# Kernel tuning notes

Hardware: AMD Instinct MI355X
Metric: run time of the kernel (lower is better)

The kernel has to match this reference:

```python
import jax, jax.numpy as jnp
import numpy as np

K = 3
KK = K * K
EPS = 1e-5


def conv2d(x, w, b, pad):
    y = jax.lax.conv_general_dilated(x, w, (1, 1), [(pad, pad), (pad, pad)],
                                     dimension_numbers=("NCHW", "OIHW", "NCHW"))
    return y + b[None, :, None, None]


def bn(x, g, b, m, v):
    inv = g / jnp.sqrt(v + EPS)
    return x * inv[None, :, None, None] + (b - m * inv)[None, :, None, None]


def deform_sample(x, dy, dx):
    # x: [B,C,H,W]; dy,dx: [B,KK,H,W] -> sampled [B,C,KK,H,W] (bilinear, zeros outside)
    B, C, H, W = x.shape
    k = jnp.arange(K, dtype=x.dtype) - 1.0  # pad=1, dilation=1, stride=1
    ky = jnp.repeat(k, K)  # [KK] row offsets
    kx = jnp.tile(k, K)    # [KK] col offsets
    hh = jnp.arange(H, dtype=x.dtype)
    ww = jnp.arange(W, dtype=x.dtype)
    py = hh[None, :, None] + ky[:, None, None] + dy  # [B,KK,H,W]
    px = ww[None, None, :] + kx[:, None, None] + dx

    def sample_one(img, py, px):
        y0f = jnp.floor(py); x0f = jnp.floor(px)
        wy = py - y0f; wx = px - x0f
        y0 = y0f.astype(jnp.int32); x0 = x0f.astype(jnp.int32)

        def gather(yi, xi, w):
            valid = (yi >= 0) & (yi < H) & (xi >= 0) & (xi < W)
            yc = jnp.clip(yi, 0, H - 1); xc = jnp.clip(xi, 0, W - 1)
            v = img[:, yc, xc]  # [C,KK,H,W]
            return v * (w * valid)[None]

        return (gather(y0, x0, (1 - wy) * (1 - wx)) +
                gather(y0, x0 + 1, (1 - wy) * wx) +
                gather(y0 + 1, x0, wy * (1 - wx)) +
                gather(y0 + 1, x0 + 1, wy * wx))

    return jax.vmap(sample_one)(x, py, px)


def setup_inputs() -> dict:
    key = jax.random.key(0)
    ks = jax.random.split(key, 16)
    B, C, H, W = 8, 256, 64, 64
    d = {
        "feature": jax.random.normal(ks[0], (B, C, H, W), jnp.float32),
        "p1_w": jax.random.normal(ks[1], (C, C, 1, 1), jnp.float32) * 0.05,
        "p1_b": jax.random.normal(ks[2], (C,), jnp.float32) * 0.05,
        "bn1_g": jax.random.normal(ks[3], (C,), jnp.float32) * 0.1 + 1.0,
        "bn1_b": jax.random.normal(ks[4], (C,), jnp.float32) * 0.05,
        "bn1_m": jax.random.normal(ks[5], (C,), jnp.float32) * 0.05,
        "bn1_v": jax.random.uniform(ks[6], (C,), jnp.float32) + 0.5,
        "off_w": jax.random.normal(ks[7], (3 * KK, 2 * C, K, K), jnp.float32) * 0.01,
        "off_b": jax.random.normal(ks[8], (3 * KK,), jnp.float32) * 0.01,
        "dcn_w": jax.random.normal(ks[9], (C, C, K, K), jnp.float32) * 0.05,
        "dcn_b": jax.random.normal(ks[10], (C,), jnp.float32) * 0.05,
        "bn2_g": jax.random.normal(ks[11], (C,), jnp.float32) * 0.1 + 1.0,
        "bn2_b": jax.random.normal(ks[12], (C,), jnp.float32) * 0.05,
        "bn2_m": jax.random.normal(ks[13], (C,), jnp.float32) * 0.05,
        "bn2_v": jax.random.uniform(ks[14], (C,), jnp.float32) + 0.5,
    }
    return d


def reference(feature, p1_w, p1_b, bn1_g, bn1_b, bn1_m, bn1_v,
              off_w, off_b, dcn_w, dcn_b, bn2_g, bn2_b, bn2_m, bn2_v):
    flipped = feature[..., ::-1]                      # flip last (W) axis
    proj = bn(conv2d(feature, p1_w, p1_b, 0), bn1_g, bn1_b, bn1_m, bn1_v)
    # DCNv2: offsets/mask from concat(flipped, proj)
    concat = jnp.concatenate([flipped, proj], axis=1)
    off = conv2d(concat, off_w, off_b, 1)             # [B,27,H,W]
    dy = off[:, :KK]
    dx = off[:, KK:2 * KK]
    mask = jax.nn.sigmoid(off[:, 2 * KK:])            # [B,KK,H,W]
    sampled = deform_sample(flipped, dy, dx)          # [B,C,KK,H,W]
    O = dcn_w.shape[0]
    y = jnp.einsum("bckhw,ock->bohw", sampled * mask[:, None], dcn_w.reshape(O, -1, KK))
    y = y + dcn_b[None, :, None, None]
    y = bn(y, bn2_g, bn2_b, bn2_m, bn2_v)
    return jax.nn.relu(proj + y)
```

## Files before the change

### kernel.cpp

```cpp
#include <hip/hip_runtime.h>
#include <hip/hip_bf16.h>
#include <math.h>

typedef __attribute__((ext_vector_type(8))) short short8;
typedef __attribute__((ext_vector_type(4))) short short4v;
typedef __attribute__((ext_vector_type(4))) float f32x4;

__device__ __forceinline__ float bs2f(short s){
    union { unsigned u; float f; } x; x.u = ((unsigned)(unsigned short)s) << 16; return x.f;
}
__device__ __forceinline__ short f2bs(float f){
    union { float f; unsigned u; } x; x.f = f;
    unsigned r = x.u + 0x7fff + ((x.u >> 16) & 1);
    return (short)(r >> 16);
}
__device__ __forceinline__ float blo(unsigned u){
    union { unsigned u; float f; } x; x.u = u << 16; return x.f;
}
__device__ __forceinline__ float bhi(unsigned u){
    union { unsigned u; float f; } x; x.u = u & 0xffff0000u; return x.f;
}
__device__ __forceinline__ unsigned pack2(float lo, float hi){
    union { float f; unsigned u; } a, b; a.f = lo; b.f = hi;
    unsigned rl = a.u + 0x7fff + ((a.u >> 16) & 1);
    unsigned rh = b.u + 0x7fff + ((b.u >> 16) & 1);
    return (rl >> 16) | (rh & 0xffff0000u);
}
__device__ __forceinline__ void gl2lds16(const void* g, void* l){
    __builtin_amdgcn_global_load_lds(
        (const __attribute__((address_space(1))) void*)g,
        (__attribute__((address_space(3))) void*)l, 16, 0, 0);
}

#define XPB ((size_t)66*66*512)


__global__ void k_prep(const float* __restrict__ p1_w, const float* __restrict__ p1_b,
                       const float* __restrict__ bn1_g, const float* __restrict__ bn1_b,
                       const float* __restrict__ bn1_m, const float* __restrict__ bn1_v,
                       const float* __restrict__ off_w,
                       const float* __restrict__ dcn_w, const float* __restrict__ dcn_b,
                       const float* __restrict__ bn2_g, const float* __restrict__ bn2_b,
                       const float* __restrict__ bn2_m, const float* __restrict__ bn2_v,
                       short* __restrict__ p1_wb, short* __restrict__ Woffb,
                       short* __restrict__ Wbf,
                       float* __restrict__ bias1f, float* __restrict__ inv2f,
                       float* __restrict__ bias2f, unsigned* __restrict__ XpadU)
{
    int blk = blockIdx.x, t = threadIdx.x;
    if (blk == 0) {
        float inv1 = bn1_g[t] / sqrtf(bn1_v[t] + 1e-5f);
        bias1f[t] = p1_b[t] * inv1 + bn1_b[t] - bn1_m[t] * inv1;
        float inv2 = bn2_g[t] / sqrtf(bn2_v[t] + 1e-5f);
        inv2f[t] = inv2;
        bias2f[t] = dcn_b[t] * inv2 + bn2_b[t] - bn2_m[t] * inv2;
    } else if (blk <= 256) {
        int ci = blk - 1;
        float inv1 = bn1_g[t] / sqrtf(bn1_v[t] + 1e-5f);
        p1_wb[t*256 + ci] = f2bs(p1_w[t*256 + ci] * inv1);
    } else if (blk <= 2560) {
        int ck = blk - 257;
        int c = ck / 9, tap = ck % 9;
        Wbf[t*2304 + tap*256 + c] = f2bs(dcn_w[t*2304 + ck]);
    } else if (blk <= 7168) {
        int e = blk - 2561;
        if (t < 32) {
            int tap = e >> 9, ci = e & 511;
            float v = off_w[((t < 27) ? t : 0)*4608 + ci*9 + tap];
            Woffb[t*4608 + e] = (t < 27) ? f2bs(v) : (short)0;
        }
    } else {
        int hb = blk - 7169;
        int b = hb / 260, i = hb % 260;
        int y, x;
        if (i < 66)       { y = 0;  x = i; }
        else if (i < 132) { y = 65; x = i - 66; }
        else { int j = i - 132; y = 1 + (j >> 1); x = (j & 1) * 65; }
        XpadU[((size_t)(b*66 + y)*66 + x)*256 + t] = 0u;
    }
}

__global__ void k_featT(const float* __restrict__ feature, short* __restrict__ Xpad)
{
    __shared__ float tile[64][65];
    int bb = blockIdx.x;
    int cg = bb & 3, h = (bb >> 2) & 63, b = bb >> 8;
    int c0 = cg * 64;
    int t = threadIdx.x;
    int lw = t & 63, li = t >> 6;
    #pragma unroll
    for (int j = 0; j < 16; ++j) {
        int cl = j*4 + li;
        tile[cl][63 - lw] = feature[((b*256 + c0 + cl)*64 + h)*64 + lw];
    }
    __syncthreads();
    #pragma unroll
    for (int j = 0; j < 16; ++j) {
        int wl = j*4 + li;
        Xpad[((size_t)(b*66 + h+1)*66 + (wl+1))*512 + c0 + lw] = f2bs(tile[lw][wl]);
    }
}

__global__ __launch_bounds__(512, 4) void k_projm(
    short* Xpad, const short* __restrict__ p1_wb, const float* __restrict__ bias1f)
{
    __shared__ short Ash[256*32];
    __shared__ short Bsh[64*32];
    int bid = blockIdx.x;
    int b = bid >> 6, h = bid & 63;
    int t = threadIdx.x;
    int lane = t & 63, w = t >> 6;
    int ln = lane & 15, q = lane >> 4;
    int r16 = lane >> 2;
    int sq  = (lane & 3) ^ ((lane >> 3) & 3);
    int rq  = (q ^ ((ln >> 1) & 3)) * 8;
    size_t rowbase = (size_t)(b*66 + h + 1)*66;

    f32x4 acc[2][4] = {};
    for (int kt = 0; kt < 8; ++kt) {
        int kcol = kt*32 + sq*8;
        #pragma unroll
        for (int i = 0; i < 2; ++i) {
            int row = w*32 + i*16 + r16;
            gl2lds16(p1_wb + (size_t)row*256 + kcol, Ash + (w*32 + i*16)*32);
        }
        if (w < 4) {
            int x = w*16 + r16;
            gl2lds16(Xpad + (rowbase + (64 - x))*512 + kcol, Bsh + (w*16)*32);
        }
        __syncthreads();
        short8 af[2], bfr[4];
        #pragma unroll
        for (int i = 0; i < 2; ++i)
            af[i] = *(const short8*)&Ash[(w*32 + i*16 + ln)*32 + rq];
        #pragma unroll
        for (int j = 0; j < 4; ++j)
            bfr[j] = *(const short8*)&Bsh[(j*16 + ln)*32 + rq];
        #pragma unroll
        for (int i = 0; i < 2; ++i)
            #pragma unroll
            for (int j = 0; j < 4; ++j)
                acc[i][j] = __builtin_amdgcn_mfma_f32_16x16x32_bf16(af[i], bfr[j], acc[i][j], 0, 0, 0);
        __syncthreads();
    }
    #pragma unroll
    for (int i = 0; i < 2; ++i) {
        int ob = w*32 + i*16 + q*4;
        #pragma unroll
        for (int j = 0; j < 4; ++j) {
            int x = j*16 + ln;
            size_t xb = (rowbase + x + 1)*512 + 256 + ob;
            short4v st;
            st.x = f2bs(acc[i][j][0] + bias1f[ob]);
            st.y = f2bs(acc[i][j][1] + bias1f[ob+1]);
            st.z = f2bs(acc[i][j][2] + bias1f[ob+2]);
            st.w = f2bs(acc[i][j][3] + bias1f[ob+3]);
            *(short4v*)&Xpad[xb] = st;
        }
    }
}

__global__ __launch_bounds__(512, 4) void k_offm(
    const short* __restrict__ Xpad, const short* __restrict__ Woffb,
    const float* __restrict__ off_b, float* __restrict__ offv)
{
    __shared__ short Ash[4][32*32];
    __shared__ short Bsh[4][64*32];
    int bid = blockIdx.x;
    int b = bid >> 6, h = bid & 63;
    int t = threadIdx.x;
    int lane = t & 63, w = t >> 6;
    int ln = lane & 15, q = lane >> 4;
    int wr = w >> 2, wc = w & 3;
    int r16 = lane >> 2;
    int sq  = (lane & 3) ^ ((lane >> 3) & 3);
    int rq  = (q ^ ((ln >> 1) & 3)) * 8;
    const short* xb = Xpad + (size_t)b*XPB;

    f32x4 acc = {};
    for (int it = 0; it < 36; ++it) {
        int tap = it >> 2, c0 = (it & 3) << 7;
        int dy = tap/3 - 1, dx = tap%3 - 1;
        #pragma unroll
        for (int s = 0; s < 4; ++s) {
            int cc = c0 + s*32 + sq*8;
            if (w < 4) {
                int row = w*16 + r16;
                const short* gB = xb + ((size_t)(h + 1 + dy)*66 + (row + dx + 1))*512 + cc;
                gl2lds16(gB, &Bsh[s][(w*16)*32]);
            } else if (w < 6) {
                int row = (w-4)*16 + r16;
                const short* gA = Woffb + (size_t)row*4608 + tap*512 + cc;
                gl2lds16(gA, &Ash[s][((w-4)*16)*32]);
            }
        }
        __syncthreads();
        #pragma unroll
        for (int s = 0; s < 4; ++s) {
            short8 af  = *(const short8*)&Ash[s][(wr*16 + ln)*32 + rq];
            short8 bfr = *(const short8*)&Bsh[s][(wc*16 + ln)*32 + rq];
            acc = __builtin_amdgcn_mfma_f32_16x16x32_bf16(af, bfr, acc, 0, 0, 0);
        }
        __syncthreads();
    }
    int x = wc*16 + ln;
    #pragma unroll
    for (int r = 0; r < 4; ++r) {
        int oc = wr*16 + q*4 + r;
        if (oc < 27)
            offv[((b*27 + oc)*64 + h)*64 + x] = acc[r] + off_b[oc];
    }
}

__global__ __launch_bounds__(512, 4) void k_gemm(
    const short* __restrict__ Xpad,
    const short* __restrict__ Wbf,
    const float* __restrict__ offv,
    const float* __restrict__ inv2f, const float* __restrict__ bias2f,
    float* __restrict__ out)
{
    __shared__ __align__(16) short Ash[2][256*32];
    __shared__ __align__(16) short Bsh[2][64*32];
    __shared__ int   c_off[576*4];
    __shared__ float c_w[576*4];
    int bid = blockIdx.x;
    int b = bid & 7, h = bid >> 3;
    int t = threadIdx.x;
    int lane = t & 63, w = t >> 6;
    int ln = lane & 15, q = lane >> 4;
    int r16 = lane >> 2;
    int sq  = (lane & 3) ^ ((lane >> 3) & 3);
    int rq  = (q ^ ((ln >> 1) & 3)) * 8;

    for (int e = t; e < 576; e += 512) {
        int p = e / 9, k = e % 9;
        int base = (b*27)*4096 + h*64 + p;
        float dy = offv[base + k*4096];
        float dx = offv[base + (9+k)*4096];
        float ms = offv[base + (18+k)*4096];
        ms = 1.f / (1.f + expf(-ms));
        float py = (float)h + (float)(k/3 - 1) + dy;
        float px = (float)p + (float)(k%3 - 1) + dx;
        float y0f = floorf(py), x0f = floorf(px);
        float wy = py - y0f, wx = px - x0f;
        int y0 = (int)y0f, x0 = (int)x0f;
        int y1 = y0 + 1, x1 = x0 + 1;
        float vy0 = (y0 >= 0 && y0 < 64) ? 1.f : 0.f;
        float vy1 = (y1 >= 0 && y1 < 64) ? 1.f : 0.f;
        float vx0 = (x0 >= 0 && x0 < 64) ? 1.f : 0.f;
        float vx1 = (x1 >= 0 && x1 < 64) ? 1.f : 0.f;
        int y0c = min(max(y0,0),63), y1c = min(max(y1,0),63);
        int x0c = min(max(x0,0),63), x1c = min(max(x1,0),63);
        c_off[e*4+0] = ((y0c+1)*66 + x0c+1)*128;
        c_off[e*4+1] = ((y0c+1)*66 + x1c+1)*128;
        c_off[e*4+2] = ((y1c+1)*66 + x0c+1)*128;
        c_off[e*4+3] = ((y1c+1)*66 + x1c+1)*128;
        c_w[e*4+0] = ms * (1.f-wy)*(1.f-wx) * vy0*vx0;
        c_w[e*4+1] = ms * (1.f-wy)*wx       * vy0*vx1;
        c_w[e*4+2] = ms * wy*(1.f-wx)       * vy1*vx0;
        c_w[e*4+3] = ms * wy*wx             * vy1*vx1;
    }
    __syncthreads();

    const uint2* fT = (const uint2*)Xpad + (size_t)b*(XPB/4);
    int pr = t >> 3;
    int jo = t & 7;
    int pe4 = pr*9*4;
    short* bdst = &Bsh[jo >> 2][pr*32 + (((jo & 3) ^ ((pr >> 1) & 3)) << 3)];

    f32x4 acc[2][4] = {};
    int4 co = *(const int4*)&c_off[pe4];
    uint4 u0 = *(const uint4*)(fT + co.x + jo*2);
    uint4 u1 = *(const uint4*)(fT + co.y + jo*2);
    uint4 u2 = *(const uint4*)(fT + co.z + jo*2);
    uint4 u3 = *(const uint4*)(fT + co.w + jo*2);

    #pragma unroll 2
    for (int kc2 = 0; kc2 < 36; ++kc2) {
        int tap = kc2 >> 2;
        int kn = kc2 < 35 ? kc2 + 1 : 35;
        int4 cn = *(const int4*)&c_off[pe4 + (kn >> 2)*4];
        int cin = ((kn & 3) << 4) + jo*2;
        uint4 v0 = *(const uint4*)(fT + cn.x + cin);
        uint4 v1 = *(const uint4*)(fT + cn.y + cin);
        uint4 v2 = *(const uint4*)(fT + cn.z + cin);
        uint4 v3 = *(const uint4*)(fT + cn.w + cin);
        #pragma unroll
        for (int s = 0; s < 2; ++s) {
            int kcol = (kc2*2 + s)*32 + sq*8;
            #pragma unroll
            for (int i = 0; i < 2; ++i) {
                int row = w*32 + i*16 + r16;
                gl2lds16(Wbf + (size_t)row*2304 + kcol, &Ash[s][(w*32 + i*16)*32]);
            }
        }
        const float4 cw = *(const float4*)&c_w[pe4 + tap*4];
        float g0 = cw.x*blo(u0.x) + cw.y*blo(u1.x) + cw.z*blo(u2.x) + cw.w*blo(u3.x);
        float g1 = cw.x*bhi(u0.x) + cw.y*bhi(u1.x) + cw.z*bhi(u2.x) + cw.w*bhi(u3.x);
        float g2 = cw.x*blo(u0.y) + cw.y*blo(u1.y) + cw.z*blo(u2.y) + cw.w*blo(u3.y);
        float g3 = cw.x*bhi(u0.y) + cw.y*bhi(u1.y) + cw.z*bhi(u2.y) + cw.w*bhi(u3.y);
        float g4 = cw.x*blo(u0.z) + cw.y*blo(u1.z) + cw.z*blo(u2.z) + cw.w*blo(u3.z);
        float g5 = cw.x*bhi(u0.z) + cw.y*bhi(u1.z) + cw.z*bhi(u2.z) + cw.w*bhi(u3.z);
        float g6 = cw.x*blo(u0.w) + cw.y*blo(u1.w) + cw.z*blo(u2.w) + cw.w*blo(u3.w);
        float g7 = cw.x*bhi(u0.w) + cw.y*bhi(u1.w) + cw.z*bhi(u2.w) + cw.w*bhi(u3.w);
        uint4 pk;
        pk.x = pack2(g0, g1); pk.y = pack2(g2, g3);
        pk.z = pack2(g4, g5); pk.w = pack2(g6, g7);
        *(uint4*)bdst = pk;
        u0 = v0; u1 = v1; u2 = v2; u3 = v3;
        __syncthreads();
        #pragma unroll
        for (int s = 0; s < 2; ++s) {
            short8 af[2], bfr[4];
            #pragma unroll
            for (int i = 0; i < 2; ++i)
                af[i] = *(const short8*)&Ash[s][(w*32 + i*16 + ln)*32 + rq];
            #pragma unroll
            for (int jj = 0; jj < 4; ++jj)
                bfr[jj] = *(const short8*)&Bsh[s][(jj*16 + ln)*32 + rq];
            #pragma unroll
            for (int i = 0; i < 2; ++i)
                #pragma unroll
                for (int jj = 0; jj < 4; ++jj)
                    acc[i][jj] = __builtin_amdgcn_mfma_f32_16x16x32_bf16(af[i], bfr[jj], acc[i][jj], 0, 0, 0);
        }
        __syncthreads();
    }

    #pragma unroll
    for (int i = 0; i < 2; ++i) {
        int ob = w*32 + i*16 + q*4;
        #pragma unroll
        for (int jj = 0; jj < 4; ++jj) {
            int p = jj*16 + ln;
            size_t xb = ((size_t)(b*66 + h + 1)*66 + p + 1)*512 + 256 + ob;
            short4v prr = *(const short4v*)&Xpad[xb];
            #pragma unroll
            for (int r = 0; r < 4; ++r) {
                int o = ob + r;
                size_t idx = ((size_t)(b*256 + o))*4096 + h*64 + p;
                float rs = bs2f(((const short*)&prr)[r]);
                float v = rs + acc[i][jj][r]*inv2f[o] + bias2f[o];
                out[idx] = v < 0.f ? 0.f : v;
            }
        }
    }
}

extern "C" void kernel_launch(void* const* d_in, const int* in_sizes, int n_in,
                              void* d_out, int out_size, void* d_ws, size_t ws_size,
                              hipStream_t stream)
{
    const float* feature = (const float*)d_in[0];
    const float* p1_w  = (const float*)d_in[1];
    const float* p1_b  = (const float*)d_in[2];
    const float* bn1_g = (const float*)d_in[3];
    const float* bn1_b = (const float*)d_in[4];
    const float* bn1_m = (const float*)d_in[5];
    const float* bn1_v = (const float*)d_in[6];
    const float* off_w = (const float*)d_in[7];
    const float* off_b = (const float*)d_in[8];
    const float* dcn_w = (const float*)d_in[9];
    const float* dcn_b = (const float*)d_in[10];
    const float* bn2_g = (const float*)d_in[11];
    const float* bn2_b = (const float*)d_in[12];
    const float* bn2_m = (const float*)d_in[13];
    const float* bn2_v = (const float*)d_in[14];

    float* ws = (float*)d_ws;
    short* Xpad   = (short*)ws;
    float* offbuf = ws + 8921088;
    short* p1_wb  = (short*)(ws + 9805824);
    short* Woffb  = (short*)(ws + 9838592);
    short* Wbf    = (short*)(ws + 9912320);
    float* bias1f = ws + 10207232;
    float* inv2f  = ws + 10207488;
    float* bias2f = ws + 10207744;

    k_prep<<<9249, 256, 0, stream>>>(p1_w, p1_b, bn1_g, bn1_b, bn1_m, bn1_v,
                                     off_w, dcn_w, dcn_b, bn2_g, bn2_b, bn2_m, bn2_v,
                                     p1_wb, Woffb, Wbf, bias1f, inv2f, bias2f,
                                     (unsigned*)Xpad);
    k_featT<<<2048, 256, 0, stream>>>(feature, Xpad);
    k_projm<<<512, 512, 0, stream>>>(Xpad, p1_wb, bias1f);
    k_offm<<<512, 512, 0, stream>>>(Xpad, Woffb, off_b, offbuf);
    k_gemm<<<512, 512, 0, stream>>>(Xpad, Wbf, offbuf, inv2f, bias2f, (float*)d_out);
}
```

Before: 234.3 us.

## Double-buffer offset conv loads and tighten deformable gather pipeline with packed offsets

In k_offm the LDS tiles are now double-buffered, so the next iteration's global-to-LDS copies are issued before the current MFMAs and one barrier per iteration is removed. In k_gemm the four bilinear corner offsets are packed into one word (base cell plus x/y step bits), which shrinks the LDS offset table and saves three LDS reads per gather. The ping-pong register buffers now use explicit waitcnt and scheduling barriers so the next gather stays in flight across the barrier, and bf16 unpack, FMA and pack use packed float2 math with the library round-to-nearest conversion. The hand-written waitcnt counts (vmcnt(4)) depend on the order the compiler emits loads, so a mismatch could cause a race or leave extra stalls.

```diff
diff --git a/kernel.cpp b/kernel.cpp
--- a/kernel.cpp
+++ b/kernel.cpp
@@ -5,6 +5,7 @@
 typedef __attribute__((ext_vector_type(8))) short short8;
 typedef __attribute__((ext_vector_type(4))) short short4v;
 typedef __attribute__((ext_vector_type(4))) float f32x4;
+typedef __attribute__((ext_vector_type(2))) float f32x2;
 
 __device__ __forceinline__ float bs2f(short s){
     union { unsigned u; float f; } x; x.u = ((unsigned)(unsigned short)s) << 16; return x.f;
@@ -14,22 +15,24 @@
     unsigned r = x.u + 0x7fff + ((x.u >> 16) & 1);
     return (short)(r >> 16);
 }
-__device__ __forceinline__ float blo(unsigned u){
-    union { unsigned u; float f; } x; x.u = u << 16; return x.f;
-}
-__device__ __forceinline__ float bhi(unsigned u){
-    union { unsigned u; float f; } x; x.u = u & 0xffff0000u; return x.f;
-}
-__device__ __forceinline__ unsigned pack2(float lo, float hi){
-    union { float f; unsigned u; } a, b; a.f = lo; b.f = hi;
-    unsigned rl = a.u + 0x7fff + ((a.u >> 16) & 1);
-    unsigned rh = b.u + 0x7fff + ((b.u >> 16) & 1);
-    return (rl >> 16) | (rh & 0xffff0000u);
+__device__ __forceinline__ f32x2 up2(unsigned u){
+    union { unsigned u; float f; } lo, hi;
+    lo.u = u << 16; hi.u = u & 0xffff0000u;
+    f32x2 r; r.x = lo.f; r.y = hi.f; return r;
+}
+__device__ __forceinline__ unsigned pk2rn(float lo, float hi){
+    __hip_bfloat162 h = __float22bfloat162_rn(make_float2(lo, hi));
+    union { __hip_bfloat162 h; unsigned u; } cv; cv.h = h; return cv.u;
 }
 __device__ __forceinline__ void gl2lds16(const void* g, void* l){
     __builtin_amdgcn_global_load_lds(
         (const __attribute__((address_space(1))) void*)g,
         (__attribute__((address_space(3))) void*)l, 16, 0, 0);
+}
+__device__ __forceinline__ void hard_barrier(){
+    __builtin_amdgcn_sched_barrier(0);
+    __builtin_amdgcn_s_barrier();
+    __builtin_amdgcn_sched_barrier(0);
 }
 
 #define XPB ((size_t)66*66*512)
@@ -164,8 +167,8 @@
     const short* __restrict__ Xpad, const short* __restrict__ Woffb,
     const float* __restrict__ off_b, float* __restrict__ offv)
 {
-    __shared__ short Ash[4][32*32];
-    __shared__ short Bsh[4][64*32];
+    __shared__ short Ash[2][4][32*32];
+    __shared__ short Bsh[2][4][64*32];
     int bid = blockIdx.x;
     int b = bid >> 6, h = bid & 63;
     int t = threadIdx.x;
@@ -177,8 +180,7 @@
     int rq  = (q ^ ((ln >> 1) & 3)) * 8;
     const short* xb = Xpad + (size_t)b*XPB;
 
-    f32x4 acc = {};
-    for (int it = 0; it < 36; ++it) {
+    auto STAGE = [&](int it, int pb){
         int tap = it >> 2, c0 = (it & 3) << 7;
         int dy = tap/3 - 1, dx = tap%3 - 1;
         #pragma unroll
@@ -187,21 +189,31 @@
             if (w < 4) {
                 int row = w*16 + r16;
                 const short* gB = xb + ((size_t)(h + 1 + dy)*66 + (row + dx + 1))*512 + cc;
-                gl2lds16(gB, &Bsh[s][(w*16)*32]);
+                gl2lds16(gB, &Bsh[pb][s][(w*16)*32]);
             } else if (w < 6) {
                 int row = (w-4)*16 + r16;
                 const short* gA = Woffb + (size_t)row*4608 + tap*512 + cc;
-                gl2lds16(gA, &Ash[s][((w-4)*16)*32]);
+                gl2lds16(gA, &Ash[pb][s][((w-4)*16)*32]);
             }
         }
-        __syncthreads();
+    };
+
+    f32x4 acc = {};
+    STAGE(0, 0);
+    asm volatile("s_waitcnt vmcnt(0)" ::: "memory");
+    hard_barrier();
+    for (int it = 0; it < 36; ++it) {
+        int pb = it & 1;
+        if (it < 35) STAGE(it + 1, pb ^ 1);
+        __builtin_amdgcn_sched_barrier(0);
         #pragma unroll
         for (int s = 0; s < 4; ++s) {
-            short8 af  = *(const short8*)&Ash[s][(wr*16 + ln)*32 + rq];
-            short8 bfr = *(const short8*)&Bsh[s][(wc*16 + ln)*32 + rq];
+            short8 af  = *(const short8*)&Ash[pb][s][(wr*16 + ln)*32 + rq];
+            short8 bfr = *(const short8*)&Bsh[pb][s][(wc*16 + ln)*32 + rq];
             acc = __builtin_amdgcn_mfma_f32_16x16x32_bf16(af, bfr, acc, 0, 0, 0);
         }
-        __syncthreads();
+        asm volatile("s_waitcnt vmcnt(0) lgkmcnt(0)" ::: "memory");
+        hard_barrier();
     }
     int x = wc*16 + ln;
     #pragma unroll
@@ -221,7 +233,7 @@
 {
     __shared__ __align__(16) short Ash[2][256*32];
     __shared__ __align__(16) short Bsh[2][64*32];
-    __shared__ int   c_off[576*4];
+    __shared__ unsigned c_pk[576];
     __shared__ float c_w[576*4];
     int bid = blockIdx.x;
     int b = bid & 7, h = bid >> 3;
@@ -251,10 +263,10 @@
         float vx1 = (x1 >= 0 && x1 < 64) ? 1.f : 0.f;
         int y0c = min(max(y0,0),63), y1c = min(max(y1,0),63);
         int x0c = min(max(x0,0),63), x1c = min(max(x1,0),63);
-        c_off[e*4+0] = ((y0c+1)*66 + x0c+1)*128;
-        c_off[e*4+1] = ((y0c+1)*66 + x1c+1)*128;
-        c_off[e*4+2] = ((y1c+1)*66 + x0c+1)*128;
-        c_off[e*4+3] = ((y1c+1)*66 + x1c+1)*128;
+        unsigned cell = (unsigned)(((y0c+1)*66 + x0c+1)*128);
+        unsigned sx = (x1c != x0c) ? 1u : 0u;
+        unsigned sy = (y1c != y0c) ? 1u : 0u;
+        c_pk[e] = cell | (sx << 20) | (sy << 21);
         c_w[e*4+0] = ms * (1.f-wy)*(1.f-wx) * vy0*vx0;
         c_w[e*4+1] = ms * (1.f-wy)*wx       * vy0*vx1;
         c_w[e*4+2] = ms * wy*(1.f-wx)       * vy1*vx0;
@@ -265,26 +277,27 @@
     const uint2* fT = (const uint2*)Xpad + (size_t)b*(XPB/4);
     int pr = t >> 3;
     int jo = t & 7;
-    int pe4 = pr*9*4;
+    int pe9 = pr*9;
     short* bdst = &Bsh[jo >> 2][pr*32 + (((jo & 3) ^ ((pr >> 1) & 3)) << 3)];
 
     f32x4 acc[2][4] = {};
-    int4 co = *(const int4*)&c_off[pe4];
-    uint4 u0 = *(const uint4*)(fT + co.x + jo*2);
-    uint4 u1 = *(const uint4*)(fT + co.y + jo*2);
-    uint4 u2 = *(const uint4*)(fT + co.z + jo*2);
-    uint4 u3 = *(const uint4*)(fT + co.w + jo*2);
-
-    #pragma unroll 2
-    for (int kc2 = 0; kc2 < 36; ++kc2) {
+    uint4 U[4], V[4];
+
+    auto GATHER = [&](int win, uint4 (&dst)[4]) {
+        unsigned pw = c_pk[pe9 + (win >> 2)];
+        int o00 = pw & 0xFFFFF;
+        int dxs = (pw >> 13) & 128;
+        int dys = ((pw >> 8) & 0x2000) | ((pw >> 13) & 0x100);
+        int cin = ((win & 3) << 4) + jo*2;
+        const uint2* p0 = fT + (o00 + cin);
+        dst[0] = *(const uint4*)(p0);
+        dst[1] = *(const uint4*)(p0 + dxs);
+        dst[2] = *(const uint4*)(p0 + dys);
+        dst[3] = *(const uint4*)(p0 + dys + dxs);
+    };
+
+    auto WIN = [&](int kc2, uint4 (&uc)[4], uint4 (&vn)[4]) {
         int tap = kc2 >> 2;
-        int kn = kc2 < 35 ? kc2 + 1 : 35;
-        int4 cn = *(const int4*)&c_off[pe4 + (kn >> 2)*4];
-        int cin = ((kn & 3) << 4) + jo*2;
-        uint4 v0 = *(const uint4*)(fT + cn.x + cin);
-        uint4 v1 = *(const uint4*)(fT + cn.y + cin);
-        uint4 v2 = *(const uint4*)(fT + cn.z + cin);
-        uint4 v3 = *(const uint4*)(fT + cn.w + cin);
         #pragma unroll
         for (int s = 0; s < 2; ++s) {
             int kcol = (kc2*2 + s)*32 + sq*8;
@@ -294,21 +307,25 @@
                 gl2lds16(Wbf + (size_t)row*2304 + kcol, &Ash[s][(w*32 + i*16)*32]);
             }
         }
-        const float4 cw = *(const float4*)&c_w[pe4 + tap*4];
-        float g0 = cw.x*blo(u0.x) + cw.y*blo(u1.x) + cw.z*blo(u2.x) + cw.w*blo(u3.x);
-        float g1 = cw.x*bhi(u0.x) + cw.y*bhi(u1.x) + cw.z*bhi(u2.x) + cw.w*bhi(u3.x);
-        float g2 = cw.x*blo(u0.y) + cw.y*blo(u1.y) + cw.z*blo(u2.y) + cw.w*blo(u3.y);
-        float g3 = cw.x*bhi(u0.y) + cw.y*bhi(u1.y) + cw.z*bhi(u2.y) + cw.w*bhi(u3.y);
-        float g4 = cw.x*blo(u0.z) + cw.y*blo(u1.z) + cw.z*blo(u2.z) + cw.w*blo(u3.z);
-        float g5 = cw.x*bhi(u0.z) + cw.y*bhi(u1.z) + cw.z*bhi(u2.z) + cw.w*bhi(u3.z);
-        float g6 = cw.x*blo(u0.w) + cw.y*blo(u1.w) + cw.z*blo(u2.w) + cw.w*blo(u3.w);
-        float g7 = cw.x*bhi(u0.w) + cw.y*bhi(u1.w) + cw.z*bhi(u2.w) + cw.w*bhi(u3.w);
-        uint4 pk;
-        pk.x = pack2(g0, g1); pk.y = pack2(g2, g3);
-        pk.z = pack2(g4, g5); pk.w = pack2(g6, g7);
-        *(uint4*)bdst = pk;
-        u0 = v0; u1 = v1; u2 = v2; u3 = v3;
-        __syncthreads();
+        __builtin_amdgcn_sched_barrier(0);
+        GATHER(kc2 < 35 ? kc2 + 1 : 35, vn);
+        const float4 cw = *(const float4*)&c_w[(pe9 + tap)*4];
+        f32x2 Wx; Wx.x = cw.x; Wx.y = cw.x;
+        f32x2 Wy; Wy.x = cw.y; Wy.y = cw.y;
+        f32x2 Wz; Wz.x = cw.z; Wz.y = cw.z;
+        f32x2 Ww; Ww.x = cw.w; Ww.y = cw.w;
+        f32x2 G0 = Wx*up2(uc[0].x) + Wy*up2(uc[1].x) + Wz*up2(uc[2].x) + Ww*up2(uc[3].x);
+        f32x2 G1 = Wx*up2(uc[0].y) + Wy*up2(uc[1].y) + Wz*up2(uc[2].y) + Ww*up2(uc[3].y);
+        f32x2 G2 = Wx*up2(uc[0].z) + Wy*up2(uc[1].z) + Wz*up2(uc[2].z) + Ww*up2(uc[3].z);
+        f32x2 G3 = Wx*up2(uc[0].w) + Wy*up2(uc[1].w) + Wz*up2(uc[2].w) + Ww*up2(uc[3].w);
+        uint4 pkv;
+        pkv.x = pk2rn(G0.x, G0.y);
+        pkv.y = pk2rn(G1.x, G1.y);
+        pkv.z = pk2rn(G2.x, G2.y);
+        pkv.w = pk2rn(G3.x, G3.y);
+        *(uint4*)bdst = pkv;
+        asm volatile("s_waitcnt vmcnt(4) lgkmcnt(0)" ::: "memory");
+        hard_barrier();
         #pragma unroll
         for (int s = 0; s < 2; ++s) {
             short8 af[2], bfr[4];
@@ -324,7 +341,14 @@
                 for (int jj = 0; jj < 4; ++jj)
                     acc[i][jj] = __builtin_amdgcn_mfma_f32_16x16x32_bf16(af[i], bfr[jj], acc[i][jj], 0, 0, 0);
         }
-        __syncthreads();
+        hard_barrier();
+    };
+
+    GATHER(0, U);
+    __builtin_amdgcn_sched_barrier(0);
+    for (int kc2 = 0; kc2 < 36; kc2 += 2) {
+        WIN(kc2, U, V);
+        WIN(kc2 + 1, V, U);
     }
 
     #pragma unroll
```

Result: no change. 235.5 us (+0.5%).
